# Kernel optimization log

Hardware: AMD Instinct MI355X
Metric: run time of the kernel (lower is better)

The kernel has to match this reference:

```python
import jax, jax.numpy as jnp
import numpy as np

NEG_SLOPE = 0.2  # PyG GATv2Conv default negative_slope


def gatv2(x, edge_index, w_l, w_r, att, bias):
    # x: [G, N, F]  (G = batch*step independent graphs sharing edge_index)
    G, N, F = x.shape
    H, C = att.shape
    # add self loops (PyG default add_self_loops=True)
    loops = jnp.arange(N, dtype=edge_index.dtype)
    src = jnp.concatenate([edge_index[0], loops])  # [E]
    dst = jnp.concatenate([edge_index[1], loops])  # [E]
    # linear projections for source / target nodes
    x_l = (x @ w_l).reshape(G, N, H, C)  # source projection
    x_r = (x @ w_r).reshape(G, N, H, C)  # target projection
    # gather along edges -> [E, G, H, C] (edge axis leading for segment ops)
    src_f = jnp.take(x_l, src, axis=1).transpose(1, 0, 2, 3)
    dst_f = jnp.take(x_r, dst, axis=1).transpose(1, 0, 2, 3)
    # GATv2 attention logit: a^T leaky_relu(W_l x_j + W_r x_i)
    e = jax.nn.leaky_relu(src_f + dst_f, NEG_SLOPE)
    logit = jnp.einsum('eghc,hc->egh', e, att)  # [E, G, H]
    # numerically-stable segment softmax over incoming edges per dst node
    m = jax.ops.segment_max(logit, dst, num_segments=N)  # [N, G, H]
    ex = jnp.exp(logit - m[dst])
    denom = jax.ops.segment_sum(ex, dst, num_segments=N)  # [N, G, H]
    alpha = ex / denom[dst]  # [E, G, H]
    # weighted scatter-add aggregation
    out = jax.ops.segment_sum(alpha[..., None] * src_f, dst, num_segments=N)  # [N,G,H,C]
    out = out.transpose(1, 0, 2, 3).reshape(G, N, H * C) + bias
    return out


def setup_inputs() -> dict:
    key = jax.random.key(0)
    ks = jax.random.split(key, 6)
    B, T, N, F = 8, 10, 1000, 64
    E, H, C = 8000, 1, 64
    x = jax.random.normal(ks[0], (B, T, N, F), dtype=jnp.float32)
    edge_index = jax.random.randint(ks[1], (2, E), 0, N, dtype=jnp.int64)
    s = 1.0 / np.sqrt(F)
    w_l = jax.random.normal(ks[2], (F, H * C), dtype=jnp.float32) * s
    w_r = jax.random.normal(ks[3], (F, H * C), dtype=jnp.float32) * s
    att = jax.random.normal(ks[4], (H, C), dtype=jnp.float32) * (1.0 / np.sqrt(C))
    bias = jnp.zeros((H * C,), dtype=jnp.float32)
    return {"x": x, "edge_index": edge_index, "w_l": w_l, "w_r": w_r, "att": att, "bias": bias}


def reference(x, edge_index, w_l, w_r, att, bias):
    B, T, N, F = x.shape
    out = gatv2(x.reshape(B * T, N, F), edge_index, w_l, w_r, att, bias)
    return out.reshape(B, T, N, -1)
```

## Files before the change

kernel.cpp:

```cpp
#include <hip/hip_runtime.h>
#include <hip/hip_bf16.h>


#define GG 80
#define NN 1000
#define EE 8000
#define MM 80000
#define NEG_SLOPE 0.2f

typedef __attribute__((ext_vector_type(8))) short short8;
typedef __attribute__((ext_vector_type(4))) float floatx4;

__device__ __forceinline__ unsigned short f2b(float f) {
    unsigned int u = __float_as_uint(f);
    unsigned int r = u + 0x7fffu + ((u >> 16) & 1u);
    return (unsigned short)(r >> 16);
}

__global__ __launch_bounds__(256) void proj_kernel(
    const float* __restrict__ x,
    const float* __restrict__ wl,
    const float* __restrict__ wr,
    unsigned short* __restrict__ XLt,
    unsigned short* __restrict__ XRt)
{
    __shared__ __align__(16) unsigned short Wt[128 * 72];
    const int t = threadIdx.x;

    for (int idx = t; idx < 8192; idx += 256) {
        int half = idx >> 12;
        int k = (idx & 4095) >> 6;
        int c = idx & 63;
        float v = half ? wr[k * 64 + c] : wl[k * 64 + c];
        Wt[(c + half * 64) * 72 + k] = f2b(v);
    }
    __syncthreads();

    const int wave = t >> 6;
    const int lane = t & 63;
    const int quad = lane >> 4;
    const int lm   = lane & 15;
    const int Rb   = (blockIdx.x * 4 + wave) * 64;

    short8 Bf[2][8];
#pragma unroll
    for (int ks = 0; ks < 2; ks++)
#pragma unroll
        for (int sub = 0; sub < 8; sub++)
            Bf[ks][sub] = *(const short8*)(&Wt[(sub * 16 + lm) * 72 + ks * 32 + quad * 8]);

    const float4* x4 = (const float4*)x;

#pragma unroll
    for (int sm = 0; sm < 4; sm++) {
        const int rbase = Rb + sm * 16;
        const int r  = rbase + lm;
        const int rc = (r < MM) ? r : (MM - 1);

        short8 Af[2];
#pragma unroll
        for (int ks = 0; ks < 2; ks++) {
            float4 p = x4[(size_t)rc * 16 + ks * 8 + quad * 2];
            float4 q = x4[(size_t)rc * 16 + ks * 8 + quad * 2 + 1];
            short8 a;
            a[0] = (short)f2b(p.x); a[1] = (short)f2b(p.y);
            a[2] = (short)f2b(p.z); a[3] = (short)f2b(p.w);
            a[4] = (short)f2b(q.x); a[5] = (short)f2b(q.y);
            a[6] = (short)f2b(q.z); a[7] = (short)f2b(q.w);
            Af[ks] = a;
        }

        floatx4 acc[8];
#pragma unroll
        for (int sub = 0; sub < 8; sub++) acc[sub] = (floatx4)(0.f);
#pragma unroll
        for (int ks = 0; ks < 2; ks++)
#pragma unroll
            for (int sub = 0; sub < 8; sub++)
                acc[sub] = __builtin_amdgcn_mfma_f32_16x16x32_bf16(Af[ks], Bf[ks][sub], acc[sub], 0, 0, 0);

#pragma unroll
        for (int reg = 0; reg < 4; reg++) {
            int rr = rbase + quad * 4 + reg;
            if (rr < MM) {
                int g = rr / 1000;
                int n = rr - g * 1000;
                size_t ob = ((size_t)n * GG + g) * 64 + lm;
#pragma unroll
                for (int sub = 0; sub < 4; sub++)
                    XLt[ob + sub * 16] = f2b(acc[sub][reg]);
#pragma unroll
                for (int sub = 4; sub < 8; sub++)
                    XRt[ob + (sub - 4) * 16] = f2b(acc[sub][reg]);
            }
        }
    }
}

__global__ __launch_bounds__(320) void agg_kernel(
    const unsigned short* __restrict__ XLt,
    const unsigned short* __restrict__ XRt,
    const int* __restrict__ ei32,
    const float* __restrict__ att,
    const float* __restrict__ bias,
    float* __restrict__ out)
{
    __shared__ int elist[256];
    __shared__ int s_cnt;
    __shared__ int s_odd;
    const int t = threadIdx.x;
    const int d = blockIdx.x;
    const int g = blockIdx.y * 40 + (t >> 3);
    const int cg = t & 7;

    if (t == 0) { s_cnt = 0; s_odd = 0; }

    float xr[8], av[8], bv[8];
    {
        const uint4 u = *(const uint4*)(XRt + ((size_t)d * GG + g) * 64 + cg * 8);
        const unsigned int uw[4] = {u.x, u.y, u.z, u.w};
#pragma unroll
        for (int q = 0; q < 4; q++) {
            xr[2 * q + 0] = __uint_as_float(uw[q] << 16);
            xr[2 * q + 1] = __uint_as_float(uw[q] & 0xffff0000u);
        }
#pragma unroll
        for (int j = 0; j < 8; j++) { av[j] = att[cg * 8 + j]; bv[j] = bias[cg * 8 + j]; }
    }

    __syncthreads();
    for (int e = t; e < 2048; e += 320)
        if (ei32[2 * e + 1] != 0) s_odd = 1;
    __syncthreads();
    const int stride = s_odd ? 1 : 2;

    for (int e = t; e < EE; e += 320) {
        int de = ei32[(size_t)(EE + e) * stride];
        if (de == d) {
            int p = atomicAdd(&s_cnt, 1);
            if (p < 255) elist[p] = ei32[(size_t)e * stride];
        }
    }
    __syncthreads();
    if (t == 0) { int c = min(s_cnt, 255); elist[c] = d; s_cnt = c + 1; }
    __syncthreads();
    const int cnt = s_cnt;

    float acc[8];
#pragma unroll
    for (int j = 0; j < 8; j++) acc[j] = 0.f;
    float dn = 0.f;

    int i = 0;
    for (; i + 3 <= cnt; i += 3) {
        int s0 = elist[i], s1 = elist[i + 1], s2 = elist[i + 2];
        uint4 u0 = *(const uint4*)(XLt + ((size_t)s0 * GG + g) * 64 + cg * 8);
        uint4 u1 = *(const uint4*)(XLt + ((size_t)s1 * GG + g) * 64 + cg * 8);
        uint4 u2 = *(const uint4*)(XLt + ((size_t)s2 * GG + g) * 64 + cg * 8);
        float xf[3][8];
        {
            const unsigned int w0[4] = {u0.x, u0.y, u0.z, u0.w};
            const unsigned int w1[4] = {u1.x, u1.y, u1.z, u1.w};
            const unsigned int w2[4] = {u2.x, u2.y, u2.z, u2.w};
#pragma unroll
            for (int q = 0; q < 4; q++) {
                xf[0][2 * q] = __uint_as_float(w0[q] << 16); xf[0][2 * q + 1] = __uint_as_float(w0[q] & 0xffff0000u);
                xf[1][2 * q] = __uint_as_float(w1[q] << 16); xf[1][2 * q + 1] = __uint_as_float(w1[q] & 0xffff0000u);
                xf[2][2 * q] = __uint_as_float(w2[q] << 16); xf[2][2 * q + 1] = __uint_as_float(w2[q] & 0xffff0000u);
            }
        }
        float p[3] = {0.f, 0.f, 0.f};
#pragma unroll
        for (int e = 0; e < 3; e++)
#pragma unroll
            for (int j = 0; j < 8; j++) {
                float v = xf[e][j] + xr[j];
                float lv = fmaxf(v, 0.f) + NEG_SLOPE * fminf(v, 0.f);
                p[e] = fmaf(av[j], lv, p[e]);
            }
#pragma unroll
        for (int m = 1; m <= 4; m <<= 1)
#pragma unroll
            for (int e = 0; e < 3; e++) p[e] += __shfl_xor(p[e], m, 64);
        float w0 = __expf(p[0]), w1 = __expf(p[1]), w2 = __expf(p[2]);
        dn += w0 + w1 + w2;
#pragma unroll
        for (int j = 0; j < 8; j++)
            acc[j] = fmaf(w2, xf[2][j], fmaf(w1, xf[1][j], fmaf(w0, xf[0][j], acc[j])));
    }
    for (; i < cnt; i++) {
        int s = elist[i];
        const uint4 u = *(const uint4*)(XLt + ((size_t)s * GG + g) * 64 + cg * 8);
        const unsigned int uw[4] = {u.x, u.y, u.z, u.w};
        float xf[8];
#pragma unroll
        for (int q = 0; q < 4; q++) {
            xf[2 * q] = __uint_as_float(uw[q] << 16);
            xf[2 * q + 1] = __uint_as_float(uw[q] & 0xffff0000u);
        }
        float p = 0.f;
#pragma unroll
        for (int j = 0; j < 8; j++) {
            float v = xf[j] + xr[j];
            float lv = fmaxf(v, 0.f) + NEG_SLOPE * fminf(v, 0.f);
            p = fmaf(av[j], lv, p);
        }
        p += __shfl_xor(p, 1, 64);
        p += __shfl_xor(p, 2, 64);
        p += __shfl_xor(p, 4, 64);
        float w = __expf(p);
        dn += w;
#pragma unroll
        for (int j = 0; j < 8; j++) acc[j] = fmaf(w, xf[j], acc[j]);
    }

    const float inv = 1.f / dn;
    float4 r0, r1;
    r0.x = acc[0] * inv + bv[0];
    r0.y = acc[1] * inv + bv[1];
    r0.z = acc[2] * inv + bv[2];
    r0.w = acc[3] * inv + bv[3];
    r1.x = acc[4] * inv + bv[4];
    r1.y = acc[5] * inv + bv[5];
    r1.z = acc[6] * inv + bv[6];
    r1.w = acc[7] * inv + bv[7];
    float* po = out + ((size_t)g * NN + d) * 64 + cg * 8;
    *(float4*)po = r0;
    *(float4*)(po + 4) = r1;
}

extern "C" void kernel_launch(void* const* d_in, const int* in_sizes, int n_in,
                              void* d_out, int out_size, void* d_ws, size_t ws_size,
                              hipStream_t stream) {
    const float* x    = (const float*)d_in[0];
    const int*   ei   = (const int*)d_in[1];
    const float* wl   = (const float*)d_in[2];
    const float* wr   = (const float*)d_in[3];
    const float* att  = (const float*)d_in[4];
    const float* bias = (const float*)d_in[5];
    float* out = (float*)d_out;

    char* ws = (char*)d_ws;
    unsigned short* XLt = (unsigned short*)ws;
    unsigned short* XRt = XLt + (size_t)NN * GG * 64;

    hipLaunchKernelGGL(proj_kernel, dim3((MM + 255) / 256), dim3(256), 0, stream,
                       x, wl, wr, XLt, XRt);
    hipLaunchKernelGGL(agg_kernel, dim3(NN, 2), dim3(320), 0, stream,
                       XLt, XRt, ei, att, bias, out);
}
```

Baseline: 129.4 us.

## Merge graph halves into one 640-thread block per node and batch edge scan

```diff
diff --git a/kernel.cpp b/kernel.cpp
--- a/kernel.cpp
+++ b/kernel.cpp
@@ -97,7 +97,7 @@
     }
 }
 
-__global__ __launch_bounds__(320) void agg_kernel(
+__global__ __launch_bounds__(640) void agg_kernel(
     const unsigned short* __restrict__ XLt,
     const unsigned short* __restrict__ XRt,
     const int* __restrict__ ei32,
@@ -107,18 +107,20 @@
 {
     __shared__ int elist[256];
     __shared__ int s_cnt;
-    __shared__ int s_odd;
     const int t = threadIdx.x;
     const int d = blockIdx.x;
-    const int g = blockIdx.y * 40 + (t >> 3);
+    const int g = t >> 3;
     const int cg = t & 7;
 
-    if (t == 0) { s_cnt = 0; s_odd = 0; }
+    if (t == 0) s_cnt = 0;
+
+    int oddw = ei32[2 * t + 1];
+    const int stride = __any(oddw != 0) ? 1 : 2;
 
     float xr[8], av[8], bv[8];
+    const uint4 uxr = *(const uint4*)(XRt + ((size_t)d * GG + g) * 64 + cg * 8);
     {
-        const uint4 u = *(const uint4*)(XRt + ((size_t)d * GG + g) * 64 + cg * 8);
-        const unsigned int uw[4] = {u.x, u.y, u.z, u.w};
+        const unsigned int uw[4] = {uxr.x, uxr.y, uxr.z, uxr.w};
 #pragma unroll
         for (int q = 0; q < 4; q++) {
             xr[2 * q + 0] = __uint_as_float(uw[q] << 16);
@@ -127,16 +129,18 @@
 #pragma unroll
         for (int j = 0; j < 8; j++) { av[j] = att[cg * 8 + j]; bv[j] = bias[cg * 8 + j]; }
     }
-
-    __syncthreads();
-    for (int e = t; e < 2048; e += 320)
-        if (ei32[2 * e + 1] != 0) s_odd = 1;
-    __syncthreads();
-    const int stride = s_odd ? 1 : 2;
-
-    for (int e = t; e < EE; e += 320) {
-        int de = ei32[(size_t)(EE + e) * stride];
-        if (de == d) {
+    __syncthreads();
+
+    int dv[13];
+#pragma unroll
+    for (int k = 0; k < 13; k++) {
+        int e = t + k * 640;
+        dv[k] = (e < EE) ? ei32[(size_t)(EE + e) * stride] : -1;
+    }
+#pragma unroll
+    for (int k = 0; k < 13; k++) {
+        if (dv[k] == d) {
+            int e = t + k * 640;
             int p = atomicAdd(&s_cnt, 1);
             if (p < 255) elist[p] = ei32[(size_t)e * stride];
         }
@@ -152,26 +156,29 @@
     float dn = 0.f;
 
     int i = 0;
-    for (; i + 3 <= cnt; i += 3) {
-        int s0 = elist[i], s1 = elist[i + 1], s2 = elist[i + 2];
+    for (; i + 4 <= cnt; i += 4) {
+        int s0 = elist[i], s1 = elist[i + 1], s2 = elist[i + 2], s3 = elist[i + 3];
         uint4 u0 = *(const uint4*)(XLt + ((size_t)s0 * GG + g) * 64 + cg * 8);
         uint4 u1 = *(const uint4*)(XLt + ((size_t)s1 * GG + g) * 64 + cg * 8);
         uint4 u2 = *(const uint4*)(XLt + ((size_t)s2 * GG + g) * 64 + cg * 8);
-        float xf[3][8];
+        uint4 u3 = *(const uint4*)(XLt + ((size_t)s3 * GG + g) * 64 + cg * 8);
+        float xf[4][8];
         {
             const unsigned int w0[4] = {u0.x, u0.y, u0.z, u0.w};
             const unsigned int w1[4] = {u1.x, u1.y, u1.z, u1.w};
             const unsigned int w2[4] = {u2.x, u2.y, u2.z, u2.w};
+            const unsigned int w3[4] = {u3.x, u3.y, u3.z, u3.w};
 #pragma unroll
             for (int q = 0; q < 4; q++) {
                 xf[0][2 * q] = __uint_as_float(w0[q] << 16); xf[0][2 * q + 1] = __uint_as_float(w0[q] & 0xffff0000u);
                 xf[1][2 * q] = __uint_as_float(w1[q] << 16); xf[1][2 * q + 1] = __uint_as_float(w1[q] & 0xffff0000u);
                 xf[2][2 * q] = __uint_as_float(w2[q] << 16); xf[2][2 * q + 1] = __uint_as_float(w2[q] & 0xffff0000u);
+                xf[3][2 * q] = __uint_as_float(w3[q] << 16); xf[3][2 * q + 1] = __uint_as_float(w3[q] & 0xffff0000u);
             }
         }
-        float p[3] = {0.f, 0.f, 0.f};
-#pragma unroll
-        for (int e = 0; e < 3; e++)
+        float p[4] = {0.f, 0.f, 0.f, 0.f};
+#pragma unroll
+        for (int e = 0; e < 4; e++)
 #pragma unroll
             for (int j = 0; j < 8; j++) {
                 float v = xf[e][j] + xr[j];
@@ -181,12 +188,12 @@
 #pragma unroll
         for (int m = 1; m <= 4; m <<= 1)
 #pragma unroll
-            for (int e = 0; e < 3; e++) p[e] += __shfl_xor(p[e], m, 64);
-        float w0 = __expf(p[0]), w1 = __expf(p[1]), w2 = __expf(p[2]);
-        dn += w0 + w1 + w2;
+            for (int e = 0; e < 4; e++) p[e] += __shfl_xor(p[e], m, 64);
+        float w0 = __expf(p[0]), w1 = __expf(p[1]), w2 = __expf(p[2]), w3 = __expf(p[3]);
+        dn += (w0 + w1) + (w2 + w3);
 #pragma unroll
         for (int j = 0; j < 8; j++)
-            acc[j] = fmaf(w2, xf[2][j], fmaf(w1, xf[1][j], fmaf(w0, xf[0][j], acc[j])));
+            acc[j] = fmaf(w3, xf[3][j], fmaf(w2, xf[2][j], fmaf(w1, xf[1][j], fmaf(w0, xf[0][j], acc[j]))));
     }
     for (; i < cnt; i++) {
         int s = elist[i];
@@ -246,6 +253,6 @@
 
     hipLaunchKernelGGL(proj_kernel, dim3((MM + 255) / 256), dim3(256), 0, stream,
                        x, wl, wr, XLt, XRt);
-    hipLaunchKernelGGL(agg_kernel, dim3(NN, 2), dim3(320), 0, stream,
+    hipLaunchKernelGGL(agg_kernel, dim3(NN), dim3(640), 0, stream,
                        XLt, XRt, ei, att, bias, out);
 }
```

Result: faster. 117.7 us (-9.1%).

## Build CSR adjacency once instead of scanning all edges per destination block

Applied to the files above, without the earlier changes.

```diff
diff --git a/kernel.cpp b/kernel.cpp
--- a/kernel.cpp
+++ b/kernel.cpp
@@ -15,6 +15,65 @@
     unsigned int u = __float_as_uint(f);
     unsigned int r = u + 0x7fffu + ((u >> 16) & 1u);
     return (unsigned short)(r >> 16);
+}
+
+__global__ __launch_bounds__(1024) void csr_kernel(
+    const int* __restrict__ ei32,
+    int* __restrict__ off,
+    int* __restrict__ list)
+{
+    __shared__ int cnt[1024];
+    __shared__ int scn[1024];
+    __shared__ int cur[1024];
+    const int t = threadIdx.x;
+
+    int oddw = ei32[2 * t + 1];
+    const int stride = __any(oddw != 0) ? 1 : 2;
+
+    cnt[t] = (t < NN) ? 1 : 0;
+    __syncthreads();
+
+    int dv[8];
+#pragma unroll
+    for (int k = 0; k < 8; k++) {
+        int e = t + (k << 10);
+        dv[k] = (e < EE) ? ei32[(size_t)(EE + e) * stride] : -1;
+    }
+#pragma unroll
+    for (int k = 0; k < 8; k++)
+        if (dv[k] >= 0) atomicAdd(&cnt[dv[k]], 1);
+    __syncthreads();
+
+    scn[t] = cnt[t];
+    __syncthreads();
+    for (int ofs = 1; ofs < 1024; ofs <<= 1) {
+        int add = (t >= ofs) ? scn[t - ofs] : 0;
+        __syncthreads();
+        scn[t] += add;
+        __syncthreads();
+    }
+    int excl = (t == 0) ? 0 : scn[t - 1];
+    if (t <= NN) off[t] = excl;
+    cur[t] = excl;
+    __syncthreads();
+
+    int sv[8];
+#pragma unroll
+    for (int k = 0; k < 8; k++) {
+        int e = t + (k << 10);
+        if (e < EE) sv[k] = ei32[(size_t)e * stride];
+    }
+#pragma unroll
+    for (int k = 0; k < 8; k++) {
+        if (dv[k] >= 0) {
+            int p = atomicAdd(&cur[dv[k]], 1);
+            list[p] = sv[k];
+        }
+    }
+    if (t < NN) {
+        int p = atomicAdd(&cur[t], 1);
+        list[p] = t;
+    }
 }
 
 __global__ __launch_bounds__(256) void proj_kernel(
@@ -97,23 +156,23 @@
     }
 }
 
-__global__ __launch_bounds__(320) void agg_kernel(
+__global__ __launch_bounds__(128) void agg_kernel(
     const unsigned short* __restrict__ XLt,
     const unsigned short* __restrict__ XRt,
-    const int* __restrict__ ei32,
+    const int* __restrict__ off,
+    const int* __restrict__ list,
     const float* __restrict__ att,
     const float* __restrict__ bias,
     float* __restrict__ out)
 {
-    __shared__ int elist[256];
-    __shared__ int s_cnt;
-    __shared__ int s_odd;
+    __shared__ int elist[128];
     const int t = threadIdx.x;
     const int d = blockIdx.x;
-    const int g = blockIdx.y * 40 + (t >> 3);
+    const int g = blockIdx.y * 16 + (t >> 3);
     const int cg = t & 7;
 
-    if (t == 0) { s_cnt = 0; s_odd = 0; }
+    const int beg = off[d];
+    const int end = off[d + 1];
 
     float xr[8], av[8], bv[8];
     {
@@ -128,90 +187,47 @@
         for (int j = 0; j < 8; j++) { av[j] = att[cg * 8 + j]; bv[j] = bias[cg * 8 + j]; }
     }
 
-    __syncthreads();
-    for (int e = t; e < 2048; e += 320)
-        if (ei32[2 * e + 1] != 0) s_odd = 1;
-    __syncthreads();
-    const int stride = s_odd ? 1 : 2;
-
-    for (int e = t; e < EE; e += 320) {
-        int de = ei32[(size_t)(EE + e) * stride];
-        if (de == d) {
-            int p = atomicAdd(&s_cnt, 1);
-            if (p < 255) elist[p] = ei32[(size_t)e * stride];
-        }
-    }
-    __syncthreads();
-    if (t == 0) { int c = min(s_cnt, 255); elist[c] = d; s_cnt = c + 1; }
-    __syncthreads();
-    const int cnt = s_cnt;
+    elist[t] = list[beg + t];
+    __syncthreads();
+    const int cnt = min(end - beg, 128);
 
     float acc[8];
 #pragma unroll
     for (int j = 0; j < 8; j++) acc[j] = 0.f;
     float dn = 0.f;
 
-    int i = 0;
-    for (; i + 3 <= cnt; i += 3) {
-        int s0 = elist[i], s1 = elist[i + 1], s2 = elist[i + 2];
-        uint4 u0 = *(const uint4*)(XLt + ((size_t)s0 * GG + g) * 64 + cg * 8);
-        uint4 u1 = *(const uint4*)(XLt + ((size_t)s1 * GG + g) * 64 + cg * 8);
-        uint4 u2 = *(const uint4*)(XLt + ((size_t)s2 * GG + g) * 64 + cg * 8);
-        float xf[3][8];
-        {
-            const unsigned int w0[4] = {u0.x, u0.y, u0.z, u0.w};
-            const unsigned int w1[4] = {u1.x, u1.y, u1.z, u1.w};
-            const unsigned int w2[4] = {u2.x, u2.y, u2.z, u2.w};
+    for (int i = 0; i < cnt; i += 8) {
+        uint4 u[8];
+#pragma unroll
+        for (int e = 0; e < 8; e++) {
+            int idx = i + e;
+            int s = elist[(idx < cnt) ? idx : 0];
+            u[e] = *(const uint4*)(XLt + ((size_t)s * GG + g) * 64 + cg * 8);
+        }
+#pragma unroll
+        for (int e = 0; e < 8; e++) {
+            const unsigned int uw[4] = {u[e].x, u[e].y, u[e].z, u[e].w};
+            float xf[8];
 #pragma unroll
             for (int q = 0; q < 4; q++) {
-                xf[0][2 * q] = __uint_as_float(w0[q] << 16); xf[0][2 * q + 1] = __uint_as_float(w0[q] & 0xffff0000u);
-                xf[1][2 * q] = __uint_as_float(w1[q] << 16); xf[1][2 * q + 1] = __uint_as_float(w1[q] & 0xffff0000u);
-                xf[2][2 * q] = __uint_as_float(w2[q] << 16); xf[2][2 * q + 1] = __uint_as_float(w2[q] & 0xffff0000u);
+                xf[2 * q]     = __uint_as_float(uw[q] << 16);
+                xf[2 * q + 1] = __uint_as_float(uw[q] & 0xffff0000u);
             }
-        }
-        float p[3] = {0.f, 0.f, 0.f};
-#pragma unroll
-        for (int e = 0; e < 3; e++)
+            float p = 0.f;
 #pragma unroll
             for (int j = 0; j < 8; j++) {
-                float v = xf[e][j] + xr[j];
+                float v = xf[j] + xr[j];
                 float lv = fmaxf(v, 0.f) + NEG_SLOPE * fminf(v, 0.f);
-                p[e] = fmaf(av[j], lv, p[e]);
+                p = fmaf(av[j], lv, p);
             }
-#pragma unroll
-        for (int m = 1; m <= 4; m <<= 1)
-#pragma unroll
-            for (int e = 0; e < 3; e++) p[e] += __shfl_xor(p[e], m, 64);
-        float w0 = __expf(p[0]), w1 = __expf(p[1]), w2 = __expf(p[2]);
-        dn += w0 + w1 + w2;
-#pragma unroll
-        for (int j = 0; j < 8; j++)
-            acc[j] = fmaf(w2, xf[2][j], fmaf(w1, xf[1][j], fmaf(w0, xf[0][j], acc[j])));
-    }
-    for (; i < cnt; i++) {
-        int s = elist[i];
-        const uint4 u = *(const uint4*)(XLt + ((size_t)s * GG + g) * 64 + cg * 8);
-        const unsigned int uw[4] = {u.x, u.y, u.z, u.w};
-        float xf[8];
-#pragma unroll
-        for (int q = 0; q < 4; q++) {
-            xf[2 * q] = __uint_as_float(uw[q] << 16);
-            xf[2 * q + 1] = __uint_as_float(uw[q] & 0xffff0000u);
-        }
-        float p = 0.f;
-#pragma unroll
-        for (int j = 0; j < 8; j++) {
-            float v = xf[j] + xr[j];
-            float lv = fmaxf(v, 0.f) + NEG_SLOPE * fminf(v, 0.f);
-            p = fmaf(av[j], lv, p);
-        }
-        p += __shfl_xor(p, 1, 64);
-        p += __shfl_xor(p, 2, 64);
-        p += __shfl_xor(p, 4, 64);
-        float w = __expf(p);
-        dn += w;
-#pragma unroll
-        for (int j = 0; j < 8; j++) acc[j] = fmaf(w, xf[j], acc[j]);
+            p += __shfl_xor(p, 1, 64);
+            p += __shfl_xor(p, 2, 64);
+            p += __shfl_xor(p, 4, 64);
+            float w = (i + e < cnt) ? __expf(p) : 0.f;
+            dn += w;
+#pragma unroll
+            for (int j = 0; j < 8; j++) acc[j] = fmaf(w, xf[j], acc[j]);
+        }
     }
 
     const float inv = 1.f / dn;
@@ -241,11 +257,14 @@
     float* out = (float*)d_out;
 
     char* ws = (char*)d_ws;
-    unsigned short* XLt = (unsigned short*)ws;
+    int* off  = (int*)ws;
+    int* list = off + 1024;
+    unsigned short* XLt = (unsigned short*)(ws + 65536);
     unsigned short* XRt = XLt + (size_t)NN * GG * 64;
 
+    hipLaunchKernelGGL(csr_kernel, dim3(1), dim3(1024), 0, stream, ei, off, list);
     hipLaunchKernelGGL(proj_kernel, dim3((MM + 255) / 256), dim3(256), 0, stream,
                        x, wl, wr, XLt, XRt);
-    hipLaunchKernelGGL(agg_kernel, dim3(NN, 2), dim3(320), 0, stream,
-                       XLt, XRt, ei, att, bias, out);
-}
+    hipLaunchKernelGGL(agg_kernel, dim3(NN, 5), dim3(128), 0, stream,
+                       XLt, XRt, off, list, att, bias, out);
+}
```

After: 117.1 us. -9.6%, faster.
